# Kernel optimization log

Hardware: AMD Instinct MI355X
Metric: run time of the kernel (lower is better)

## Reference

```python
import jax, jax.numpy as jnp
import numpy as np

N = 4096
N_FEAT = 1024
N_HID = 8
N_HEADS = 8
N_CLASSES = 16
ALPHA = 0.2
NEG_BIG = -9e15


def setup_inputs() -> dict:
    key = jax.random.key(0)
    ks = jax.random.split(key, 6)
    x = jax.random.normal(ks[0], (N, N_FEAT), dtype=jnp.float32)
    adj = (jax.random.uniform(ks[1], (N, N)) < 0.01).astype(jnp.float32)
    adj = jnp.maximum(adj, jnp.eye(N, dtype=jnp.float32))
    W_heads = jax.random.normal(ks[2], (N_HEADS, N_FEAT, N_HID), dtype=jnp.float32) * 0.05
    a_heads = jax.random.normal(ks[3], (N_HEADS, 2 * N_HID, 1), dtype=jnp.float32) * 0.05
    W_final = jax.random.normal(ks[4], (N_HEADS * N_HID, N_CLASSES), dtype=jnp.float32) * 0.05
    a_final = jax.random.normal(ks[5], (2 * N_CLASSES, 1), dtype=jnp.float32) * 0.05
    return {"x": x, "adj": adj, "W_heads": W_heads, "a_heads": a_heads,
            "W_final": W_final, "a_final": a_final}


def gat_layer(h, adj, W, a):
    # h: [N, Fin], W: [Fin, Fout], a: [2*Fout, 1]
    Wh = h @ W                                  # [N, Fout]
    Fout = W.shape[1]
    f_src = Wh @ a[:Fout, 0]                    # [N] -- Wh_i . a[:F]
    f_dst = Wh @ a[Fout:, 0]                    # [N] -- Wh_j . a[F:]
    e = jax.nn.leaky_relu(f_src[:, None] + f_dst[None, :], ALPHA)  # [N, N]
    e = jnp.where(adj > 0, e, NEG_BIG)
    attention = jax.nn.softmax(e, axis=1)       # dropout skipped (eval mode)
    return attention @ Wh                        # [N, Fout]


def reference(x, adj, W_heads, a_heads, W_final, a_final):
    # multi-head GAT layer (8 independent heads), concat along features
    heads = jax.vmap(lambda W, a: gat_layer(x, adj, W, a))(W_heads, a_heads)  # [H, N, n_hid]
    h = jnp.transpose(heads, (1, 0, 2)).reshape(x.shape[0], -1)               # [N, H*n_hid]
    h = jax.nn.elu(h)
    out = gat_layer(h, adj, W_final, a_final)    # [N, n_classes]
    return jax.nn.log_softmax(out, axis=1)
```

## Files before the change

### kernel.cpp

```cpp
#include <hip/hip_runtime.h>
#include <math.h>

#define N 4096
#define NFEAT 1024
#define NHID 8
#define NHEADS 8
#define NCLS 16
#define CAP 128

__global__ __launch_bounds__(256) void k0_wt(const float* __restrict__ W_heads,
                                             float* __restrict__ Wt) {
    int t = blockIdx.x * 256 + threadIdx.x;
    int f = t >> 6, c = t & 63;
    Wt[t] = W_heads[(c >> 3) * (NFEAT * NHID) + f * NHID + (c & 7)];
}

__global__ __launch_bounds__(256) void k1_gemm(const float* __restrict__ x,
                                               const float* __restrict__ Wt,
                                               const float* __restrict__ a_heads,
                                               float* __restrict__ Wh,
                                               float* __restrict__ fsrc,
                                               float* __restrict__ fdst) {
    __shared__ float xs[8 * NFEAT];
    __shared__ float red[4][8][64];
    const int tid = threadIdx.x;
    const int w = tid >> 6, c = tid & 63;
    const int row0 = blockIdx.x * 8;

    const float4* xg = (const float4*)(x + (size_t)row0 * NFEAT);
    float4* xls = (float4*)xs;
    #pragma unroll
    for (int i = 0; i < 8; ++i) xls[tid + i * 256] = xg[tid + i * 256];
    __syncthreads();

    float acc[8] = {};
    const float* wp = Wt + (size_t)(w * 256) * 64 + c;
    const float* xw = xs + w * 256;
    for (int k = 0; k < 256; k += 8) {
        float wv[8];
        #pragma unroll
        for (int u = 0; u < 8; ++u) wv[u] = wp[(k + u) * 64];
        #pragma unroll
        for (int r = 0; r < 8; ++r) {
            const float4 a0 = *(const float4*)(xw + r * NFEAT + k);
            const float4 a1 = *(const float4*)(xw + r * NFEAT + k + 4);
            acc[r] += a0.x * wv[0] + a0.y * wv[1] + a0.z * wv[2] + a0.w * wv[3]
                    + a1.x * wv[4] + a1.y * wv[5] + a1.z * wv[6] + a1.w * wv[7];
        }
    }
    #pragma unroll
    for (int r = 0; r < 8; ++r) red[w][r][c] = acc[r];
    __syncthreads();
    #pragma unroll
    for (int e0 = 0; e0 < 2; ++e0) {
        int e = tid + e0 * 256;
        int r = e >> 6, cc = e & 63;
        float v = red[0][r][cc] + red[1][r][cc] + red[2][r][cc] + red[3][r][cc];
        Wh[(size_t)(row0 + r) * 64 + cc] = v;
        int h = cc >> 3, kh = cc & 7;
        float vs = v * a_heads[h * 16 + kh];
        float vd = v * a_heads[h * 16 + 8 + kh];
        vs += __shfl_xor(vs, 1); vs += __shfl_xor(vs, 2); vs += __shfl_xor(vs, 4);
        vd += __shfl_xor(vd, 1); vd += __shfl_xor(vd, 2); vd += __shfl_xor(vd, 4);
        if (kh == 0) { fsrc[h * N + row0 + r] = vs; fdst[h * N + row0 + r] = vd; }
    }
}

__global__ __launch_bounds__(256) void k3_csr(const float* __restrict__ adj,
                                              int* __restrict__ deg,
                                              int* __restrict__ nbr) {
    __shared__ int cnt;
    const int row = blockIdx.x;
    if (threadIdx.x == 0) cnt = 0;
    __syncthreads();
    const float4* arow = (const float4*)(adj + (size_t)row * N);
    int* out = nbr + (size_t)row * CAP;
    for (int b = threadIdx.x; b < N / 4; b += 256) {
        float4 v = arow[b];
        if (v.x > 0.f) { int p = atomicAdd(&cnt, 1); if (p < CAP) out[p] = b * 4 + 0; }
        if (v.y > 0.f) { int p = atomicAdd(&cnt, 1); if (p < CAP) out[p] = b * 4 + 1; }
        if (v.z > 0.f) { int p = atomicAdd(&cnt, 1); if (p < CAP) out[p] = b * 4 + 2; }
        if (v.w > 0.f) { int p = atomicAdd(&cnt, 1); if (p < CAP) out[p] = b * 4 + 3; }
    }
    __syncthreads();
    if (threadIdx.x == 0) deg[row] = cnt > CAP ? CAP : cnt;
}

__global__ __launch_bounds__(256) void k4_attn1(const float* __restrict__ fsrc,
                                                const float* __restrict__ fdst,
                                                const float* __restrict__ Wh,
                                                const int* __restrict__ deg,
                                                const int* __restrict__ nbr,
                                                const float* __restrict__ W_final,
                                                const float* __restrict__ a_final,
                                                float* __restrict__ Wh2,
                                                float* __restrict__ fsrc2,
                                                float* __restrict__ fdst2) {
    __shared__ float hrow[4][64];
    const int wave = threadIdx.x >> 6;
    const int lane = threadIdx.x & 63;
    const int row = blockIdx.x * 4 + wave;
    const int h = lane >> 3;
    const int d = deg[row];
    const int* nl = nbr + (size_t)row * CAP;
    const float fs = fsrc[h * N + row];
    const float* fd = fdst + h * N;

    float s = 0.f, acc = 0.f;
    int n = 0;
    for (; n + 4 <= d; n += 4) {
        int j0 = nl[n], j1 = nl[n + 1], j2 = nl[n + 2], j3 = nl[n + 3];
        float e0 = fs + fd[j0], e1 = fs + fd[j1], e2 = fs + fd[j2], e3 = fs + fd[j3];
        float v0 = Wh[(size_t)j0 * 64 + lane], v1 = Wh[(size_t)j1 * 64 + lane];
        float v2 = Wh[(size_t)j2 * 64 + lane], v3 = Wh[(size_t)j3 * 64 + lane];
        float w0 = __expf(fmaxf(e0, 0.2f * e0));
        float w1 = __expf(fmaxf(e1, 0.2f * e1));
        float w2 = __expf(fmaxf(e2, 0.2f * e2));
        float w3 = __expf(fmaxf(e3, 0.2f * e3));
        s += (w0 + w1) + (w2 + w3);
        acc += w0 * v0 + w1 * v1 + w2 * v2 + w3 * v3;
    }
    for (; n < d; ++n) {
        int j = nl[n];
        float e = fs + fd[j];
        float wgt = __expf(fmaxf(e, 0.2f * e));
        s += wgt;
        acc += wgt * Wh[(size_t)j * 64 + lane];
    }
    float o = acc / s;
    o = o > 0.f ? o : (__expf(o) - 1.f);
    hrow[wave][lane] = o;
    __syncthreads();

    const int g = lane >> 4, cc = lane & 15;
    float p = 0.f;
    #pragma unroll
    for (int f0 = 0; f0 < 16; ++f0) {
        int f = g * 16 + f0;
        p += hrow[wave][f] * W_final[f * 16 + cc];
    }
    p += __shfl_xor(p, 16);
    p += __shfl_xor(p, 32);
    if (g == 0) Wh2[(size_t)row * 16 + cc] = p;
    float vs = p * a_final[cc];
    float vd = p * a_final[16 + cc];
    #pragma unroll
    for (int mm = 1; mm < 16; mm <<= 1) {
        vs += __shfl_xor(vs, mm);
        vd += __shfl_xor(vd, mm);
    }
    if (lane == 0) { fsrc2[row] = vs; fdst2[row] = vd; }
}

__global__ __launch_bounds__(256) void k6_attn2(const float* __restrict__ fsrc2,
                                                const float* __restrict__ fdst2,
                                                const float* __restrict__ Wh2,
                                                const int* __restrict__ deg,
                                                const int* __restrict__ nbr,
                                                float* __restrict__ out) {
    const int wave = threadIdx.x >> 6;
    const int lane = threadIdx.x & 63;
    const int row = blockIdx.x * 4 + wave;
    const int jj = lane >> 4, c = lane & 15;
    const int d = deg[row];
    const int* nl = nbr + (size_t)row * CAP;
    const float fs = fsrc2[row];

    float s = 0.f, acc = 0.f;
    for (int n = jj; n < d; n += 4) {
        int j = nl[n];
        float e = fs + fdst2[j];
        float w = __expf(fmaxf(e, 0.2f * e));
        s += w;
        acc += w * Wh2[(size_t)j * 16 + c];
    }
    s += __shfl_xor(s, 16);  s += __shfl_xor(s, 32);
    acc += __shfl_xor(acc, 16); acc += __shfl_xor(acc, 32);

    float u = acc / s;
    float m2 = u;
    #pragma unroll
    for (int mm = 1; mm < 16; mm <<= 1) m2 = fmaxf(m2, __shfl_xor(m2, mm));
    float tv = u - m2;
    float se = __expf(tv);
    #pragma unroll
    for (int mm = 1; mm < 16; mm <<= 1) se += __shfl_xor(se, mm);
    float o = tv - logf(se);
    if (jj == 0) out[(size_t)row * 16 + c] = o;
}

extern "C" void kernel_launch(void* const* d_in, const int* in_sizes, int n_in,
                              void* d_out, int out_size, void* d_ws, size_t ws_size,
                              hipStream_t stream) {
    const float* x       = (const float*)d_in[0];
    const float* adj     = (const float*)d_in[1];
    const float* W_heads = (const float*)d_in[2];
    const float* a_heads = (const float*)d_in[3];
    const float* W_final = (const float*)d_in[4];
    const float* a_final = (const float*)d_in[5];
    float* out = (float*)d_out;

    float* ws    = (float*)d_ws;
    float* Wh    = ws;
    float* fsrc  = Wh + 262144;
    float* fdst  = fsrc + 32768;
    float* Wh2   = fdst + 32768;
    float* fsrc2 = Wh2 + 65536;
    float* fdst2 = fsrc2 + 4096;
    int*   deg   = (int*)(fdst2 + 4096);
    int*   nbr   = deg + 4096;
    float* Wt    = (float*)(nbr + 4096 * CAP);

    k3_csr  <<<N,    256, 0, stream>>>(adj, deg, nbr);
    k0_wt   <<<(NFEAT * 64) / 256, 256, 0, stream>>>(W_heads, Wt);
    k1_gemm <<<512,  256, 0, stream>>>(x, Wt, a_heads, Wh, fsrc, fdst);
    k4_attn1<<<N/4,  256, 0, stream>>>(fsrc, fdst, Wh, deg, nbr,
                                       W_final, a_final, Wh2, fsrc2, fdst2);
    k6_attn2<<<N/4,  256, 0, stream>>>(fsrc2, fdst2, Wh2, deg, nbr, out);
}
```

Measured before the change: 146.8 us.

## Fuse adjacency scan and feature GEMM into one launch, drop W transpose

Merges the CSR adjacency scan and the head-projection GEMM into a single kernel, using block index to split work: the first 512 blocks do the GEMM and the remaining 4096 blocks scan adjacency rows. The separate weight-transpose kernel is removed and the GEMM reads W_heads directly with a stride-8 layout. This cuts two kernel launches and lets the bandwidth-bound scan overlap with the compute-bound GEMM. In exchange, the scan blocks now reserve the GEMM's large shared-memory footprint, which can limit their occupancy, and the direct W reads are less coalesced.

New measurement: 137.7 us. -6.2%, faster.

```diff
diff --git a/kernel.cpp b/kernel.cpp
--- a/kernel.cpp
+++ b/kernel.cpp
@@ -8,22 +8,45 @@
 #define NCLS 16
 #define CAP 128
 
-__global__ __launch_bounds__(256) void k0_wt(const float* __restrict__ W_heads,
-                                             float* __restrict__ Wt) {
-    int t = blockIdx.x * 256 + threadIdx.x;
-    int f = t >> 6, c = t & 63;
-    Wt[t] = W_heads[(c >> 3) * (NFEAT * NHID) + f * NHID + (c & 7)];
-}
-
-__global__ __launch_bounds__(256) void k1_gemm(const float* __restrict__ x,
-                                               const float* __restrict__ Wt,
-                                               const float* __restrict__ a_heads,
-                                               float* __restrict__ Wh,
-                                               float* __restrict__ fsrc,
-                                               float* __restrict__ fdst) {
-    __shared__ float xs[8 * NFEAT];
-    __shared__ float red[4][8][64];
+#define GEMM_BLOCKS 512
+
+__global__ __launch_bounds__(256) void ka_scan_gemm(const float* __restrict__ adj,
+                                                    const float* __restrict__ x,
+                                                    const float* __restrict__ W_heads,
+                                                    const float* __restrict__ a_heads,
+                                                    int* __restrict__ deg,
+                                                    int* __restrict__ nbr,
+                                                    float* __restrict__ Wh,
+                                                    float* __restrict__ fsrc,
+                                                    float* __restrict__ fdst) {
+    __shared__ float smem[8 * NFEAT + 4 * 8 * 64];
     const int tid = threadIdx.x;
+
+    if (blockIdx.x >= GEMM_BLOCKS) {
+        const int row = blockIdx.x - GEMM_BLOCKS;
+        int* cnt = (int*)smem;
+        if (tid == 0) *cnt = 0;
+        __syncthreads();
+        const float4* arow = (const float4*)(adj + (size_t)row * N);
+        int* outl = nbr + (size_t)row * CAP;
+        float4 v[4];
+        #pragma unroll
+        for (int i = 0; i < 4; ++i) v[i] = arow[tid + i * 256];
+        #pragma unroll
+        for (int i = 0; i < 4; ++i) {
+            const int b = (tid + i * 256) * 4;
+            if (v[i].x > 0.f) { int p = atomicAdd(cnt, 1); if (p < CAP) outl[p] = b + 0; }
+            if (v[i].y > 0.f) { int p = atomicAdd(cnt, 1); if (p < CAP) outl[p] = b + 1; }
+            if (v[i].z > 0.f) { int p = atomicAdd(cnt, 1); if (p < CAP) outl[p] = b + 2; }
+            if (v[i].w > 0.f) { int p = atomicAdd(cnt, 1); if (p < CAP) outl[p] = b + 3; }
+        }
+        __syncthreads();
+        if (tid == 0) deg[row] = *cnt > CAP ? CAP : *cnt;
+        return;
+    }
+
+    float* xs = smem;
+    float (*red)[8][64] = (float (*)[8][64])(smem + 8 * NFEAT);
     const int w = tid >> 6, c = tid & 63;
     const int row0 = blockIdx.x * 8;
 
@@ -34,12 +57,13 @@
     __syncthreads();
 
     float acc[8] = {};
-    const float* wp = Wt + (size_t)(w * 256) * 64 + c;
+    const float* wp = W_heads + (size_t)(c >> 3) * (NFEAT * NHID) + (c & 7)
+                    + (size_t)(w * 256) * NHID;
     const float* xw = xs + w * 256;
     for (int k = 0; k < 256; k += 8) {
         float wv[8];
         #pragma unroll
-        for (int u = 0; u < 8; ++u) wv[u] = wp[(k + u) * 64];
+        for (int u = 0; u < 8; ++u) wv[u] = wp[(k + u) * 8];
         #pragma unroll
         for (int r = 0; r < 8; ++r) {
             const float4 a0 = *(const float4*)(xw + r * NFEAT + k);
@@ -66,27 +90,7 @@
     }
 }
 
-__global__ __launch_bounds__(256) void k3_csr(const float* __restrict__ adj,
-                                              int* __restrict__ deg,
-                                              int* __restrict__ nbr) {
-    __shared__ int cnt;
-    const int row = blockIdx.x;
-    if (threadIdx.x == 0) cnt = 0;
-    __syncthreads();
-    const float4* arow = (const float4*)(adj + (size_t)row * N);
-    int* out = nbr + (size_t)row * CAP;
-    for (int b = threadIdx.x; b < N / 4; b += 256) {
-        float4 v = arow[b];
-        if (v.x > 0.f) { int p = atomicAdd(&cnt, 1); if (p < CAP) out[p] = b * 4 + 0; }
-        if (v.y > 0.f) { int p = atomicAdd(&cnt, 1); if (p < CAP) out[p] = b * 4 + 1; }
-        if (v.z > 0.f) { int p = atomicAdd(&cnt, 1); if (p < CAP) out[p] = b * 4 + 2; }
-        if (v.w > 0.f) { int p = atomicAdd(&cnt, 1); if (p < CAP) out[p] = b * 4 + 3; }
-    }
-    __syncthreads();
-    if (threadIdx.x == 0) deg[row] = cnt > CAP ? CAP : cnt;
-}
-
-__global__ __launch_bounds__(256) void k4_attn1(const float* __restrict__ fsrc,
+__global__ __launch_bounds__(256) void kb_attn1(const float* __restrict__ fsrc,
                                                 const float* __restrict__ fdst,
                                                 const float* __restrict__ Wh,
                                                 const int* __restrict__ deg,
@@ -152,7 +156,7 @@
     if (lane == 0) { fsrc2[row] = vs; fdst2[row] = vd; }
 }
 
-__global__ __launch_bounds__(256) void k6_attn2(const float* __restrict__ fsrc2,
+__global__ __launch_bounds__(256) void kc_attn2(const float* __restrict__ fsrc2,
                                                 const float* __restrict__ fdst2,
                                                 const float* __restrict__ Wh2,
                                                 const int* __restrict__ deg,
@@ -209,12 +213,10 @@
     float* fdst2 = fsrc2 + 4096;
     int*   deg   = (int*)(fdst2 + 4096);
     int*   nbr   = deg + 4096;
-    float* Wt    = (float*)(nbr + 4096 * CAP);
-
-    k3_csr  <<<N,    256, 0, stream>>>(adj, deg, nbr);
-    k0_wt   <<<(NFEAT * 64) / 256, 256, 0, stream>>>(W_heads, Wt);
-    k1_gemm <<<512,  256, 0, stream>>>(x, Wt, a_heads, Wh, fsrc, fdst);
-    k4_attn1<<<N/4,  256, 0, stream>>>(fsrc, fdst, Wh, deg, nbr,
-                                       W_final, a_final, Wh2, fsrc2, fdst2);
-    k6_attn2<<<N/4,  256, 0, stream>>>(fsrc2, fdst2, Wh2, deg, nbr, out);
-}
+
+    ka_scan_gemm<<<GEMM_BLOCKS + N, 256, 0, stream>>>(adj, x, W_heads, a_heads,
+                                                      deg, nbr, Wh, fsrc, fdst);
+    kb_attn1    <<<N / 4, 256, 0, stream>>>(fsrc, fdst, Wh, deg, nbr,
+                                            W_final, a_final, Wh2, fsrc2, fdst2);
+    kc_attn2    <<<N / 4, 256, 0, stream>>>(fsrc2, fdst2, Wh2, deg, nbr, out);
+}
```
